# Performance work log

Hardware: AMD Instinct MI355X
Metric: run time of the kernel (lower is better)

Reference implementation:

```python
import jax, jax.numpy as jnp
import numpy as np

B, S, T, E, H = 64, 128, 128, 1024, 1024
NEG = -1e9  # masked-score fill


def setup_inputs() -> dict:
    key = jax.random.key(0)
    ks = jax.random.split(key, 10)
    sd = lambda k, shape, fan: (jax.random.normal(k, shape, jnp.float32) * (fan ** -0.5))
    return {
        "trg_embed": jax.random.normal(ks[0], (B, T, E), jnp.float32),
        "encoder_hidden": jax.random.normal(ks[1], (B, S, 2 * H), jnp.float32),
        "encoder_final": jax.random.normal(ks[2], (1, B, 2 * H), jnp.float32),
        "src_mask": jnp.ones((B, 1, S), bool),
        "trg_mask": jnp.ones((B, T), bool),
        "W_bridge": sd(ks[3], (H, 2 * H), 2 * H),
        "b_bridge": jnp.zeros((H,), jnp.float32),
        "W_key": sd(ks[4], (H, 2 * H), 2 * H),
        "W_query": sd(ks[5], (H, H), H),
        "W_energy": sd(ks[6], (1, H), H),
        "W_ih": sd(ks[7], (3 * H, E + 2 * H), E + 2 * H),
        "W_hh": sd(ks[8], (3 * H, H), H),
        "b_ih": jnp.zeros((3 * H,), jnp.float32),
        "b_hh": jnp.zeros((3 * H,), jnp.float32),
        "W_pre": sd(ks[9], (2 * H, E + 3 * H), E + 3 * H),
    }


def _decode(trg_embed, encoder_hidden, encoder_final, src_mask,
            W_bridge, b_bridge, W_key, W_query, W_energy,
            W_ih, W_hh, b_ih, b_hh, W_pre):
    # init_hidden: tanh(bridge(encoder_final))  -> [num_layers=1, B, H]
    h0 = jnp.tanh(encoder_final @ W_bridge.T + b_bridge)
    # proj_key computed once over the source  -> [B, S, H]
    proj_key = encoder_hidden @ W_key.T
    mask = src_mask[:, 0, :]  # [B, S]
    Hd = W_hh.shape[1]

    def step(hidden, x_t):  # hidden: [1,B,H], x_t: [B,E]
        h = hidden[-1]
        # Bahdanau attention
        q = h @ W_query.T                                   # [B,H]
        scores = jnp.tanh(q[:, None, :] + proj_key) @ W_energy[0]  # [B,S]
        scores = jnp.where(mask, scores, NEG)
        alphas = jax.nn.softmax(scores, axis=-1)
        context = jnp.einsum('bs,bsd->bd', alphas, encoder_hidden)  # [B,2H]
        # GRU cell (PyTorch gate math)
        x = jnp.concatenate([x_t, context], axis=-1)        # [B, E+2H]
        gi = x @ W_ih.T + b_ih
        gh = h @ W_hh.T + b_hh
        r = jax.nn.sigmoid(gi[:, :Hd] + gh[:, :Hd])
        z = jax.nn.sigmoid(gi[:, Hd:2 * Hd] + gh[:, Hd:2 * Hd])
        n = jnp.tanh(gi[:, 2 * Hd:] + r * gh[:, 2 * Hd:])
        h_new = (1.0 - z) * n + z * h
        # pre-output (dropout is identity in eval)
        pre = jnp.concatenate([x_t, h_new, context], axis=-1) @ W_pre.T  # [B,2H]
        return h_new[None], (h_new, pre)

    hidden_final, (outs, pres) = jax.lax.scan(step, h0, jnp.swapaxes(trg_embed, 0, 1))
    decoder_states = jnp.swapaxes(outs, 0, 1)       # [B,T,H]
    pre_output_vectors = jnp.swapaxes(pres, 0, 1)   # [B,T,2H]
    return decoder_states, hidden_final, pre_output_vectors


def reference(trg_embed, encoder_hidden, encoder_final, src_mask, trg_mask,
              W_bridge, b_bridge, W_key, W_query, W_energy,
              W_ih, W_hh, b_ih, b_hh, W_pre):
    # trg_mask only determines max_len, which equals trg_embed.shape[1] here
    return _decode(trg_embed, encoder_hidden, encoder_final, src_mask,
                   W_bridge, b_bridge, W_key, W_query, W_energy,
                   W_ih, W_hh, b_ih, b_hh, W_pre)
```

## Files before the change

kernel.cpp:

```cpp
#include <hip/hip_runtime.h>
#include <hip/hip_bf16.h>

typedef short    bf16x8 __attribute__((ext_vector_type(8)));
typedef float    f32x4  __attribute__((ext_vector_type(4)));
typedef unsigned short u16x8 __attribute__((ext_vector_type(8)));

#define B_  64
#define S_  128
#define T_  128
#define E_  1024
#define H_  1024
#define NBLK 256

#define RLX __ATOMIC_RELAXED
#define AGT __HIP_MEMORY_SCOPE_AGENT

__device__ __forceinline__ unsigned short f2bf(float f) {
    unsigned u = __float_as_uint(f);
    unsigned r = (u + 0x7FFFu + ((u >> 16) & 1u)) >> 16;
    return (unsigned short)r;
}
__device__ __forceinline__ float bf2f(unsigned short u) {
    return __uint_as_float((unsigned)u << 16);
}
__device__ __forceinline__ float my_tanh(float x) {
    float e = __expf(2.0f * x);
    return 1.0f - 2.0f / (e + 1.0f);
}
__device__ __forceinline__ float my_sig(float x) {
    return 1.0f / (1.0f + __expf(-x));
}

__device__ __forceinline__ void st8c(void* p, unsigned long long v) {
    __hip_atomic_store((unsigned long long*)p, v, RLX, AGT);
}
__device__ __forceinline__ unsigned long long ld8c(const void* p) {
    return __hip_atomic_load((const unsigned long long*)p, RLX, AGT);
}
__device__ __forceinline__ void st4c(void* p, unsigned v) {
    __hip_atomic_store((unsigned*)p, v, RLX, AGT);
}
__device__ __forceinline__ void st4f(void* p, float v) {
    __hip_atomic_store((float*)p, v, RLX, AGT);
}
__device__ __forceinline__ float ld4f(const void* p) {
    return __hip_atomic_load((const float*)p, RLX, AGT);
}

__device__ __forceinline__ void gld_lds16(const void* g, void* l) {
    __builtin_amdgcn_global_load_lds(
        (const __attribute__((address_space(1))) unsigned int*)(unsigned long long)g,
        (__attribute__((address_space(3))) unsigned int*)(unsigned int)(unsigned long long)l,
        16, 0, 0);
}

__device__ __forceinline__ void gbar(int* sync, int g, int ord) {
    __syncthreads();
    if (threadIdx.x == 0) {
        int* lc = sync + 64 + (g >> 3) * 64;
        int* lg = lc + 32;
        if (__hip_atomic_fetch_add(lc, 1, RLX, AGT) == 8 * ord - 1) {
            if (__hip_atomic_fetch_add(sync, 1, RLX, AGT) == 32 * ord - 1) {
                __hip_atomic_store(sync + 32, ord, RLX, AGT);
            } else {
                while (__hip_atomic_load(sync + 32, RLX, AGT) < ord)
                    __builtin_amdgcn_s_sleep(2);
            }
            __hip_atomic_store(lg, ord, RLX, AGT);
        } else {
            while (__hip_atomic_load(lg, RLX, AGT) < ord)
                __builtin_amdgcn_s_sleep(2);
        }
    }
    __syncthreads();
}

__global__ void k_cvt(const float* __restrict__ s, unsigned short* __restrict__ d, long n) {
    long i = ((long)blockIdx.x * blockDim.x + threadIdx.x) * 4;
    if (i >= n) return;
    float4 f = *(const float4*)(s + i);
    ushort4 o;
    o.x = f2bf(f.x); o.y = f2bf(f.y); o.z = f2bf(f.z); o.w = f2bf(f.w);
    *(ushort4*)(d + i) = o;
}

__global__ void k_cvt_te(const float* __restrict__ s, unsigned short* __restrict__ d, long n) {
    long i = ((long)blockIdx.x * blockDim.x + threadIdx.x) * 4;
    if (i >= n) return;
    float4 f = *(const float4*)(s + i);
    long row = i >> 10, col = i & 1023;
    ushort4 o;
    o.x = f2bf(f.x); o.y = f2bf(f.y); o.z = f2bf(f.z); o.w = f2bf(f.w);
    *(ushort4*)(d + row * 4096 + col) = o;
}

template<int OUTBF>
__global__ __launch_bounds__(256) void k_gemm(const unsigned short* __restrict__ A, long lda,
                                              const unsigned short* __restrict__ W, long ldw,
                                              void* __restrict__ Cv, long ldc, int K) {
    const int lane = threadIdx.x & 63;
    const int wv   = threadIdx.x >> 6;
    const int r    = lane & 15, g = lane >> 4;
    const long m0  = (long)blockIdx.y * 64 + wv * 16;
    const long n0  = (long)blockIdx.x * 64;
    const unsigned short* a  = A + (m0 + r) * lda + g * 8;
    const unsigned short* w0 = W + (n0 + r) * ldw + g * 8;
    f32x4 acc[4] = {};
    for (int k = 0; k < K; k += 32) {
        bf16x8 av = *(const bf16x8*)(a + k);
#pragma unroll
        for (int j = 0; j < 4; ++j) {
            bf16x8 bv = *(const bf16x8*)(w0 + (long)j * 16 * ldw + k);
            acc[j] = __builtin_amdgcn_mfma_f32_16x16x32_bf16(av, bv, acc[j], 0, 0, 0);
        }
    }
#pragma unroll
    for (int j = 0; j < 4; ++j) {
        long row = m0 + g * 4;
        long col = n0 + j * 16 + r;
#pragma unroll
        for (int rr = 0; rr < 4; ++rr) {
            float v = acc[j][rr];
            if (OUTBF) ((unsigned short*)Cv)[(row + rr) * ldc + col] = f2bf(v);
            else       ((float*)Cv)[(row + rr) * ldc + col] = v;
        }
    }
}

template<int OUTBF>
__global__ __launch_bounds__(256) void k_gemm128(const unsigned short* __restrict__ A, long lda,
                                                 const unsigned short* __restrict__ W, long ldw,
                                                 void* __restrict__ Cv, long ldc, int K) {
    __shared__ unsigned short lA[128 * 32];
    __shared__ unsigned short lB[128 * 32];
    const int tid  = threadIdx.x;
    const int lane = tid & 63, wv = tid >> 6;
    const int r = lane & 15, gg = lane >> 4;
    const int wm = (wv >> 1) * 64, wn = (wv & 1) * 64;
    const long m0 = (long)blockIdx.y * 128;
    const long n0 = (long)blockIdx.x * 128;
    const int c0 = 2 * wv, c1 = 2 * wv + 1;
    const int ra0 = c0 * 16 + (lane >> 2);
    const int ra1 = c1 * 16 + (lane >> 2);
    const int cb8 = (lane & 3) * 8;
    const unsigned short* a0 = A + (m0 + ra0) * lda + cb8;
    const unsigned short* a1 = A + (m0 + ra1) * lda + cb8;
    const unsigned short* b0 = W + (n0 + ra0) * ldw + cb8;
    const unsigned short* b1 = W + (n0 + ra1) * ldw + cb8;
    f32x4 acc[4][4] = {};
    for (int k0 = 0; k0 < K; k0 += 32) {
        __syncthreads();
        gld_lds16(a0 + k0, &lA[c0 * 512]);
        gld_lds16(a1 + k0, &lA[c1 * 512]);
        gld_lds16(b0 + k0, &lB[c0 * 512]);
        gld_lds16(b1 + k0, &lB[c1 * 512]);
        __syncthreads();
        bf16x8 av[4], bv[4];
#pragma unroll
        for (int i = 0; i < 4; ++i) {
            av[i] = *(const bf16x8*)&lA[(wm + i * 16 + r) * 32 + gg * 8];
            bv[i] = *(const bf16x8*)&lB[(wn + i * 16 + r) * 32 + gg * 8];
        }
#pragma unroll
        for (int mi = 0; mi < 4; ++mi)
#pragma unroll
            for (int ni = 0; ni < 4; ++ni)
                acc[mi][ni] = __builtin_amdgcn_mfma_f32_16x16x32_bf16(av[mi], bv[ni], acc[mi][ni], 0, 0, 0);
    }
#pragma unroll
    for (int mi = 0; mi < 4; ++mi) {
#pragma unroll
        for (int ni = 0; ni < 4; ++ni) {
            const long col = n0 + wn + ni * 16 + r;
#pragma unroll
            for (int rr = 0; rr < 4; ++rr) {
                const long row = m0 + wm + mi * 16 + gg * 4 + rr;
                float v = acc[mi][ni][rr];
                if (OUTBF) ((unsigned short*)Cv)[row * ldc + col] = f2bf(v);
                else       ((float*)Cv)[row * ldc + col] = v;
            }
        }
    }
}

__global__ void k_h0act(const float* __restrict__ hp, const float* __restrict__ bb,
                        float* __restrict__ h, unsigned short* __restrict__ hbf) {
    int i = blockIdx.x * 256 + threadIdx.x;
    float v = my_tanh(hp[i] + bb[i & 1023]);
    h[i] = v; hbf[i] = f2bf(v);
}

__global__ __launch_bounds__(1024) void k_steps(
        const unsigned short* __restrict__ pk, const unsigned short* __restrict__ eh,
        const unsigned short* __restrict__ whp, const unsigned short* __restrict__ wih,
        const float* __restrict__ We, const float* __restrict__ gix,
        const float* __restrict__ bih, const float* __restrict__ bhh,
        const float* __restrict__ h0f, const unsigned short* __restrict__ hbf,
        float* __restrict__ hp, unsigned short* __restrict__ preC,
        float* __restrict__ o_states, float* __restrict__ o_hf,
        int* __restrict__ sync, float* __restrict__ scb) {
    __shared__ unsigned short ehs[S_ * 512];
    __shared__ float smf[16 * 64 * 4];
    __shared__ unsigned short hsm[256];
    const int g    = blockIdx.x;
    const int tid  = threadIdx.x;
    const int wv   = tid >> 6, lane = tid & 63;
    const int r    = lane & 15, gg = lane >> 4;

    const int p1_bq = g & 3, p1_cb = g >> 2;
    const int p1_ct = wv & 3, p1_ks = wv >> 2;
    const int p2_b  = (g & 7) * 8 + (g >> 5);
    const int p2_q4 = (g >> 3) & 3;
    const int jt = g >> 2, bg = g & 3;
    const int j0 = jt * 16, b0 = bg * 16;
    const int lr = tid >> 4, lc = tid & 15;
    float hreg = (tid < 256) ? h0f[(long)(b0 + lr) * 1024 + j0 + lc] : 0.f;

    {
        const unsigned short* src = eh + (long)p2_b * S_ * 2048 + p2_q4 * 512;
#pragma unroll
        for (int it = 0; it < 8; ++it) {
            int i = it * 1024 + tid;
            int row = i >> 6, c8i = (i & 63) * 8;
            *(u16x8*)&ehs[row * 512 + c8i] = *(const u16x8*)(src + (long)row * 2048 + c8i);
        }
    }
    __syncthreads();

    int ord = 0;

#pragma unroll 1
    for (int t = 0; t < T_; ++t) {
        {
            const int n0 = p1_cb * 64 + p1_ct * 16;
            const int k0 = p1_ks * 256;
            const int b  = p1_bq * 16 + r;
            const unsigned short* arow = (t == 0)
                ? hbf + (long)b * 1024 + k0 + gg * 8
                : preC + ((long)b * T_ + (t - 1)) * 4096 + 1024 + k0 + gg * 8;
            const unsigned short* bw = whp + (long)(n0 + r) * 1024 + k0 + gg * 8;
            f32x4 acc = {};
#pragma unroll
            for (int k = 0; k < 256; k += 32) {
                bf16x8 av = *(const bf16x8*)(arow + k);
                bf16x8 bv = *(const bf16x8*)(bw + k);
                acc = __builtin_amdgcn_mfma_f32_16x16x32_bf16(av, bv, acc, 0, 0, 0);
            }
            *(f32x4*)&smf[(wv * 64 + lane) * 4] = acc;
            __syncthreads();
            if (p1_ks == 0) {
                f32x4 s0 = *(f32x4*)&smf[((0 * 4 + p1_ct) * 64 + lane) * 4];
                f32x4 s1 = *(f32x4*)&smf[((1 * 4 + p1_ct) * 64 + lane) * 4];
                f32x4 s2 = *(f32x4*)&smf[((2 * 4 + p1_ct) * 64 + lane) * 4];
                f32x4 s3 = *(f32x4*)&smf[((3 * 4 + p1_ct) * 64 + lane) * 4];
                f32x4 s = s0 + s1 + s2 + s3;
#pragma unroll
                for (int rr = 0; rr < 4; ++rr)
                    st4f(&hp[(long)(p1_bq * 16 + gg * 4 + rr) * 4096 + n0 + r], s[rr]);
            }
        }
        gbar(sync, g, ++ord);

        {
            const int b = p2_b;
            const int hh = lane * 16;
            float q[16], w16[16];
#pragma unroll
            for (int i = 0; i < 8; ++i) {
                unsigned long long u = ld8c(hp + (long)b * 4096 + hh + 2 * i);
                q[2 * i]     = __uint_as_float((unsigned)u);
                q[2 * i + 1] = __uint_as_float((unsigned)(u >> 32));
            }
#pragma unroll
            for (int i = 0; i < 16; ++i) w16[i] = We[hh + i];
#pragma unroll
            for (int k2 = 0; k2 < 2; ++k2) {
                const int s = p2_q4 * 32 + wv * 2 + k2;
                const unsigned short* row = pk + ((long)b * S_ + s) * 1024 + hh;
                u16x8 v0 = *(const u16x8*)(row);
                u16x8 v1 = *(const u16x8*)(row + 8);
                float acc = 0.f;
#pragma unroll
                for (int i = 0; i < 8; ++i) acc += my_tanh(q[i] + bf2f(v0[i])) * w16[i];
#pragma unroll
                for (int i = 0; i < 8; ++i) acc += my_tanh(q[8 + i] + bf2f(v1[i])) * w16[8 + i];
#pragma unroll
                for (int off = 32; off; off >>= 1) acc += __shfl_xor(acc, off);
                if (lane == 0) st4f(&scb[b * 128 + s], acc);
            }
            __syncthreads();
            if (tid == 0) {
                int* bc = sync + 4096 + b * 32;
                __hip_atomic_fetch_add(bc, 1, RLX, AGT);
                while (__hip_atomic_load(bc, RLX, AGT) < 4 * (t + 1))
                    __builtin_amdgcn_s_sleep(2);
            }
            __syncthreads();
            float* red = &smf[648];
            float e = 0.f, sc = 0.f;
            if (tid < 128) {
                sc = ld4f(&scb[b * 128 + tid]);
                float m = sc;
#pragma unroll
                for (int off = 32; off; off >>= 1) m = fmaxf(m, __shfl_xor(m, off));
                if ((tid & 63) == 0) red[tid >> 6] = m;
            }
            __syncthreads();
            if (tid < 128) {
                float M = fmaxf(red[0], red[1]);
                e = __expf(sc - M);
                float s = e;
#pragma unroll
                for (int off = 32; off; off >>= 1) s += __shfl_xor(s, off);
                if ((tid & 63) == 0) red[2 + (tid >> 6)] = s;
            }
            __syncthreads();
            if (tid < 128) smf[512 + tid] = e / (red[2] + red[3]);
            __syncthreads();
            const int cp = tid & 255, sseg = tid >> 8;
            const unsigned short* ehp = ehs + (sseg * 32) * 512 + cp * 2;
            float a0 = 0.f, a1 = 0.f;
#pragma unroll 4
            for (int s2 = 0; s2 < 32; ++s2) {
                float alv = smf[512 + sseg * 32 + s2];
                ushort2 v = *(const ushort2*)(ehp + s2 * 512);
                a0 += alv * bf2f(v.x); a1 += alv * bf2f(v.y);
            }
            smf[1024 + (sseg * 256 + cp) * 2]     = a0;
            smf[1024 + (sseg * 256 + cp) * 2 + 1] = a1;
            __syncthreads();
            if (tid < 256) {
                float b0s = smf[1024 + tid * 2]         + smf[1024 + (256 + tid) * 2]
                          + smf[1024 + (512 + tid) * 2] + smf[1024 + (768 + tid) * 2];
                float b1s = smf[1024 + tid * 2 + 1]         + smf[1024 + (256 + tid) * 2 + 1]
                          + smf[1024 + (512 + tid) * 2 + 1] + smf[1024 + (768 + tid) * 2 + 1];
                unsigned pack = (unsigned)f2bf(b0s) | ((unsigned)f2bf(b1s) << 16);
                st4c(preC + ((long)b * T_ + t) * 4096 + 2048 + p2_q4 * 512 + tid * 2, pack);
            }
        }
        gbar(sync, g, ++ord);

        {
            if (wv < 12) {
                const int c = wv >> 2, ks = wv & 3, k0 = ks * 512;
                const unsigned short* ar = preC + ((long)(b0 + r) * T_ + t) * 4096 + 2048 + k0 + gg * 8;
                const unsigned short* bw = wih + ((long)(c * 1024 + j0 + r)) * 3072 + 1024 + k0 + gg * 8;
                f32x4 acc = {};
#pragma unroll
                for (int k = 0; k < 512; k += 32) {
                    bf16x8 av = *(const bf16x8*)(ar + k);
                    bf16x8 bv = *(const bf16x8*)(bw + k);
                    acc = __builtin_amdgcn_mfma_f32_16x16x32_bf16(av, bv, acc, 0, 0, 0);
                }
                *(f32x4*)&smf[(wv * 64 + lane) * 4] = acc;
            }
            __syncthreads();
            if (tid < 256) {
                const int lane_ = (lr >> 2) * 16 + lc, rr_ = lr & 3;
                float gi[3];
#pragma unroll
                for (int c = 0; c < 3; ++c) {
                    gi[c] = smf[((c * 4 + 0) * 64 + lane_) * 4 + rr_]
                          + smf[((c * 4 + 1) * 64 + lane_) * 4 + rr_]
                          + smf[((c * 4 + 2) * 64 + lane_) * 4 + rr_]
                          + smf[((c * 4 + 3) * 64 + lane_) * 4 + rr_];
                }
                const int b = b0 + lr, j = j0 + lc;
                const long bt = (long)b * T_ + t;
                float ghr = ld4f(&hp[(long)b * 4096 + 1024 + j]);
                float ghz = ld4f(&hp[(long)b * 4096 + 2048 + j]);
                float ghn = ld4f(&hp[(long)b * 4096 + 3072 + j]);
                float grv = gix[bt * 3072 + j]        + gi[0] + bih[j]        + ghr + bhh[j];
                float gzv = gix[bt * 3072 + 1024 + j] + gi[1] + bih[1024 + j] + ghz + bhh[1024 + j];
                float gni = gix[bt * 3072 + 2048 + j] + gi[2] + bih[2048 + j];
                float ghn2 = ghn + bhh[2048 + j];
                float rg = my_sig(grv);
                float zg = my_sig(gzv);
                float nv = my_tanh(gni + rg * ghn2);
                float hn = (1.f - zg) * nv + zg * hreg;
                hreg = hn;
                unsigned short hb16 = f2bf(hn);
                o_states[bt * 1024 + j] = hn;
                if (t == T_ - 1) o_hf[(long)b * 1024 + j] = hn;
                hsm[tid] = hb16;
            }
            __syncthreads();
            if (tid < 64) {
                const int plr = tid >> 2, pc4 = (tid & 3) * 4;
                unsigned long long v =
                      (unsigned long long)hsm[plr * 16 + pc4]
                    | ((unsigned long long)hsm[plr * 16 + pc4 + 1] << 16)
                    | ((unsigned long long)hsm[plr * 16 + pc4 + 2] << 32)
                    | ((unsigned long long)hsm[plr * 16 + pc4 + 3] << 48);
                st8c(preC + ((long)(b0 + plr) * T_ + t) * 4096 + 1024 + j0 + pc4, v);
            }
        }
        gbar(sync, g, ++ord);
    }
}

extern "C" void kernel_launch(void* const* d_in, const int* in_sizes, int n_in,
                              void* d_out, int out_size, void* d_ws, size_t ws_size,
                              hipStream_t stream) {
    const float* te  = (const float*)d_in[0];
    const float* eh  = (const float*)d_in[1];
    const float* ef  = (const float*)d_in[2];
    const float* Wb  = (const float*)d_in[5];
    const float* bb  = (const float*)d_in[6];
    const float* Wk  = (const float*)d_in[7];
    const float* Wq  = (const float*)d_in[8];
    const float* We  = (const float*)d_in[9];
    const float* Wih = (const float*)d_in[10];
    const float* Whh = (const float*)d_in[11];
    const float* bih = (const float*)d_in[12];
    const float* bhh = (const float*)d_in[13];
    const float* Wpre= (const float*)d_in[14];

    char* ws = (char*)d_ws;
    if (ws_size < 272236544UL) return;
    float*          h0f   = (float*)(ws + 0);
    float*          hp    = (float*)(ws + 262144);
    unsigned short* hbf   = (unsigned short*)(ws + 1310720);
    unsigned short* efb   = (unsigned short*)(ws + 1441792);
    int*            syncb = (int*)(ws + 1441792 + 65536);
    float*          scb   = (float*)(ws + 1572864);
    unsigned short* ehb   = (unsigned short*)(ws + 1703936);
    unsigned short* pkb   = (unsigned short*)(ws + 35258368);
    unsigned short* preC  = (unsigned short*)(ws + 52035584);
    float*          gix   = (float*)(ws + 119144448);
    unsigned short* wbb   = (unsigned short*)(ws + 219807744);
    unsigned short* wkb   = (unsigned short*)(ws + 224002048);
    unsigned short* whpb  = (unsigned short*)(ws + 228196352);
    unsigned short* wihb  = (unsigned short*)(ws + 236584960);
    unsigned short* wpreb = (unsigned short*)(ws + 255459328);

    float* o_states = (float*)d_out;
    float* o_hf     = o_states + (long)B_ * T_ * H_;
    float* o_pre    = o_hf + (long)B_ * H_;

    auto cvt = [&](const float* s, unsigned short* d, long n) {
        k_cvt<<<dim3((unsigned)((n / 4 + 255) / 256)), 256, 0, stream>>>(s, d, n);
    };
    cvt(eh,  ehb,  (long)B_ * S_ * 2048);
    cvt(ef,  efb,  (long)B_ * 2048);
    cvt(Wb,  wbb,  1024L * 2048);
    cvt(Wk,  wkb,  1024L * 2048);
    cvt(Wq,  whpb, 1024L * 1024);
    cvt(Whh, whpb + 1024L * 1024, 3072L * 1024);
    cvt(Wih, wihb, 3072L * 3072);
    cvt(Wpre,wpreb,2048L * 4096);
    k_cvt_te<<<8192, 256, 0, stream>>>(te, preC, (long)B_ * T_ * 1024);

    k_gemm<0><<<dim3(16, 1), 256, 0, stream>>>(efb, 2048, wbb, 2048, hp, 1024, 2048);
    k_h0act<<<256, 256, 0, stream>>>(hp, bb, h0f, hbf);
    (void)hipMemsetAsync(syncb, 0, 32768, stream);
    k_gemm128<1><<<dim3(8, 64), 256, 0, stream>>>(ehb, 2048, wkb, 2048, pkb, 1024, 2048);
    k_gemm128<0><<<dim3(24, 64), 256, 0, stream>>>(preC, 4096, wihb, 3072, gix, 3072, 1024);

    k_steps<<<NBLK, 1024, 0, stream>>>(pkb, ehb, whpb, wihb, We, gix, bih, bhh,
                                       h0f, hbf, hp, preC, o_states, o_hf, syncb, scb);

    k_gemm128<0><<<dim3(16, 64), 256, 0, stream>>>(preC, 4096, wpreb, 4096, o_pre, 2048, 4096);
}
```

Measured before the change: 5.467 ms.

## Split query and W_hh projections, replace grid barrier with per-batch-group flags

Phase 1 now runs only the query projection (h@W_query) on 64 blocks and writes it to a small qbuf. Each block then signals a per-batch-group counter instead of entering a full grid barrier. The recurrent W_hh gate products move into the GRU phase, where spare waves 12-14 compute them locally over the full K=1024. This removes one global barrier per step and the hp round-trip for the gh terms. In exchange, a few waves per block do a longer serial MFMA loop, and attention blocks spin-wait on counters.

```diff
diff --git a/kernel.cpp b/kernel.cpp
--- a/kernel.cpp
+++ b/kernel.cpp
@@ -196,7 +196,7 @@
         const float* __restrict__ We, const float* __restrict__ gix,
         const float* __restrict__ bih, const float* __restrict__ bhh,
         const float* __restrict__ h0f, const unsigned short* __restrict__ hbf,
-        float* __restrict__ hp, unsigned short* __restrict__ preC,
+        float* __restrict__ qbuf, unsigned short* __restrict__ preC,
         float* __restrict__ o_states, float* __restrict__ o_hf,
         int* __restrict__ sync, float* __restrict__ scb) {
     __shared__ unsigned short ehs[S_ * 512];
@@ -207,8 +207,8 @@
     const int wv   = tid >> 6, lane = tid & 63;
     const int r    = lane & 15, gg = lane >> 4;
 
-    const int p1_bq = g & 3, p1_cb = g >> 2;
-    const int p1_ct = wv & 3, p1_ks = wv >> 2;
+    const int p1_bq = g >> 4, p1_ct = g & 15;
+    const int p1_nt = wv & 3, p1_ks = wv >> 2;
     const int p2_b  = (g & 7) * 8 + (g >> 5);
     const int p2_q4 = (g >> 3) & 3;
     const int jt = g >> 2, bg = g & 3;
@@ -231,8 +231,8 @@
 
 #pragma unroll 1
     for (int t = 0; t < T_; ++t) {
-        {
-            const int n0 = p1_cb * 64 + p1_ct * 16;
+        if (g < 64) {
+            const int n0 = p1_ct * 64 + p1_nt * 16;
             const int k0 = p1_ks * 256;
             const int b  = p1_bq * 16 + r;
             const unsigned short* arow = (t == 0)
@@ -249,25 +249,33 @@
             *(f32x4*)&smf[(wv * 64 + lane) * 4] = acc;
             __syncthreads();
             if (p1_ks == 0) {
-                f32x4 s0 = *(f32x4*)&smf[((0 * 4 + p1_ct) * 64 + lane) * 4];
-                f32x4 s1 = *(f32x4*)&smf[((1 * 4 + p1_ct) * 64 + lane) * 4];
-                f32x4 s2 = *(f32x4*)&smf[((2 * 4 + p1_ct) * 64 + lane) * 4];
-                f32x4 s3 = *(f32x4*)&smf[((3 * 4 + p1_ct) * 64 + lane) * 4];
+                f32x4 s0 = *(f32x4*)&smf[((0 * 4 + p1_nt) * 64 + lane) * 4];
+                f32x4 s1 = *(f32x4*)&smf[((1 * 4 + p1_nt) * 64 + lane) * 4];
+                f32x4 s2 = *(f32x4*)&smf[((2 * 4 + p1_nt) * 64 + lane) * 4];
+                f32x4 s3 = *(f32x4*)&smf[((3 * 4 + p1_nt) * 64 + lane) * 4];
                 f32x4 s = s0 + s1 + s2 + s3;
 #pragma unroll
                 for (int rr = 0; rr < 4; ++rr)
-                    st4f(&hp[(long)(p1_bq * 16 + gg * 4 + rr) * 4096 + n0 + r], s[rr]);
-            }
-        }
-        gbar(sync, g, ++ord);
+                    st4f(&qbuf[(long)(p1_bq * 16 + gg * 4 + rr) * 1024 + n0 + r], s[rr]);
+            }
+            __syncthreads();
+            if (tid == 0)
+                __hip_atomic_fetch_add(sync + 6656 + p1_bq * 32, 1, RLX, AGT);
+        }
 
         {
             const int b = p2_b;
+            if (tid == 0) {
+                int* qc = sync + 6656 + (b >> 4) * 32;
+                while (__hip_atomic_load(qc, RLX, AGT) < 16 * (t + 1))
+                    __builtin_amdgcn_s_sleep(2);
+            }
+            __syncthreads();
             const int hh = lane * 16;
             float q[16], w16[16];
 #pragma unroll
             for (int i = 0; i < 8; ++i) {
-                unsigned long long u = ld8c(hp + (long)b * 4096 + hh + 2 * i);
+                unsigned long long u = ld8c(qbuf + (long)b * 1024 + hh + 2 * i);
                 q[2 * i]     = __uint_as_float((unsigned)u);
                 q[2 * i + 1] = __uint_as_float((unsigned)(u >> 32));
             }
@@ -353,27 +361,39 @@
                     acc = __builtin_amdgcn_mfma_f32_16x16x32_bf16(av, bv, acc, 0, 0, 0);
                 }
                 *(f32x4*)&smf[(wv * 64 + lane) * 4] = acc;
+            } else if (wv < 15) {
+                const int c = wv - 12;
+                const unsigned short* ar = (t == 0)
+                    ? hbf + (long)(b0 + r) * 1024 + gg * 8
+                    : preC + ((long)(b0 + r) * T_ + (t - 1)) * 4096 + 1024 + gg * 8;
+                const unsigned short* bw = whp + (long)(1024 + c * 1024 + j0 + r) * 1024 + gg * 8;
+                f32x4 acc = {};
+#pragma unroll 4
+                for (int k = 0; k < 1024; k += 32) {
+                    bf16x8 av = *(const bf16x8*)(ar + k);
+                    bf16x8 bv = *(const bf16x8*)(bw + k);
+                    acc = __builtin_amdgcn_mfma_f32_16x16x32_bf16(av, bv, acc, 0, 0, 0);
+                }
+                *(f32x4*)&smf[(wv * 64 + lane) * 4] = acc;
             }
             __syncthreads();
             if (tid < 256) {
                 const int lane_ = (lr >> 2) * 16 + lc, rr_ = lr & 3;
-                float gi[3];
+                float gi[3], gh[3];
 #pragma unroll
                 for (int c = 0; c < 3; ++c) {
                     gi[c] = smf[((c * 4 + 0) * 64 + lane_) * 4 + rr_]
                           + smf[((c * 4 + 1) * 64 + lane_) * 4 + rr_]
                           + smf[((c * 4 + 2) * 64 + lane_) * 4 + rr_]
                           + smf[((c * 4 + 3) * 64 + lane_) * 4 + rr_];
+                    gh[c] = smf[((12 + c) * 64 + lane_) * 4 + rr_];
                 }
                 const int b = b0 + lr, j = j0 + lc;
                 const long bt = (long)b * T_ + t;
-                float ghr = ld4f(&hp[(long)b * 4096 + 1024 + j]);
-                float ghz = ld4f(&hp[(long)b * 4096 + 2048 + j]);
-                float ghn = ld4f(&hp[(long)b * 4096 + 3072 + j]);
-                float grv = gix[bt * 3072 + j]        + gi[0] + bih[j]        + ghr + bhh[j];
-                float gzv = gix[bt * 3072 + 1024 + j] + gi[1] + bih[1024 + j] + ghz + bhh[1024 + j];
+                float grv = gix[bt * 3072 + j]        + gi[0] + bih[j]        + gh[0] + bhh[j];
+                float gzv = gix[bt * 3072 + 1024 + j] + gi[1] + bih[1024 + j] + gh[1] + bhh[1024 + j];
                 float gni = gix[bt * 3072 + 2048 + j] + gi[2] + bih[2048 + j];
-                float ghn2 = ghn + bhh[2048 + j];
+                float ghn2 = gh[2] + bhh[2048 + j];
                 float rg = my_sig(grv);
                 float zg = my_sig(gzv);
                 float nv = my_tanh(gni + rg * ghn2);
```

Result: slower. 6.059 ms (+10.8%).

## Split persistent-kernel grid barrier into independent per-batch-quarter barriers

Applied to the files above, without the earlier changes.

Reassigns the 256 persistent blocks so that each group of 64 blocks handles one 16-row batch quarter in every phase (hidden projection, attention, GRU update). The full-grid barrier becomes a 64-block barrier per batch quarter, with its own counters, so the quarters advance through time steps independently. This is meant to shrink barrier fan-in and let slower quarters avoid stalling the whole grid. The block-to-data mapping also groups blocks by XCD index, and the sync buffer clear is doubled to cover the extra counters.

```diff
diff --git a/kernel.cpp b/kernel.cpp
--- a/kernel.cpp
+++ b/kernel.cpp
@@ -47,32 +47,32 @@
     return __hip_atomic_load((const float*)p, RLX, AGT);
 }
 
+__device__ __forceinline__ void gbarq(int* s, int leaf, int ord) {
+    __syncthreads();
+    if (threadIdx.x == 0) {
+        int* lc = s + 64 + leaf * 64;
+        int* lg = lc + 32;
+        if (__hip_atomic_fetch_add(lc, 1, RLX, AGT) == 8 * ord - 1) {
+            if (__hip_atomic_fetch_add(s, 1, RLX, AGT) == 8 * ord - 1) {
+                __hip_atomic_store(s + 32, ord, RLX, AGT);
+            } else {
+                while (__hip_atomic_load(s + 32, RLX, AGT) < ord)
+                    __builtin_amdgcn_s_sleep(2);
+            }
+            __hip_atomic_store(lg, ord, RLX, AGT);
+        } else {
+            while (__hip_atomic_load(lg, RLX, AGT) < ord)
+                __builtin_amdgcn_s_sleep(2);
+        }
+    }
+    __syncthreads();
+}
+
 __device__ __forceinline__ void gld_lds16(const void* g, void* l) {
     __builtin_amdgcn_global_load_lds(
         (const __attribute__((address_space(1))) unsigned int*)(unsigned long long)g,
         (__attribute__((address_space(3))) unsigned int*)(unsigned int)(unsigned long long)l,
         16, 0, 0);
-}
-
-__device__ __forceinline__ void gbar(int* sync, int g, int ord) {
-    __syncthreads();
-    if (threadIdx.x == 0) {
-        int* lc = sync + 64 + (g >> 3) * 64;
-        int* lg = lc + 32;
-        if (__hip_atomic_fetch_add(lc, 1, RLX, AGT) == 8 * ord - 1) {
-            if (__hip_atomic_fetch_add(sync, 1, RLX, AGT) == 32 * ord - 1) {
-                __hip_atomic_store(sync + 32, ord, RLX, AGT);
-            } else {
-                while (__hip_atomic_load(sync + 32, RLX, AGT) < ord)
-                    __builtin_amdgcn_s_sleep(2);
-            }
-            __hip_atomic_store(lg, ord, RLX, AGT);
-        } else {
-            while (__hip_atomic_load(lg, RLX, AGT) < ord)
-                __builtin_amdgcn_s_sleep(2);
-        }
-    }
-    __syncthreads();
 }
 
 __global__ void k_cvt(const float* __restrict__ s, unsigned short* __restrict__ d, long n) {
@@ -207,12 +207,15 @@
     const int wv   = tid >> 6, lane = tid & 63;
     const int r    = lane & 15, gg = lane >> 4;
 
-    const int p1_bq = g & 3, p1_cb = g >> 2;
+    const int bq  = g >> 6, z = g & 63;
+    const int xcd = z & 7, sub = z >> 3;
+    int* bqs = sync + bq * 1024;
+    const int p1_cb = xcd * 8 + sub;
     const int p1_ct = wv & 3, p1_ks = wv >> 2;
-    const int p2_b  = (g & 7) * 8 + (g >> 5);
-    const int p2_q4 = (g >> 3) & 3;
-    const int jt = g >> 2, bg = g & 3;
-    const int j0 = jt * 16, b0 = bg * 16;
+    const int p2_b  = bq * 16 + xcd * 2 + (sub & 1);
+    const int p2_q4 = sub >> 1;
+    const int jt = xcd * 8 + sub;
+    const int j0 = jt * 16, b0 = bq * 16;
     const int lr = tid >> 4, lc = tid & 15;
     float hreg = (tid < 256) ? h0f[(long)(b0 + lr) * 1024 + j0 + lc] : 0.f;
 
@@ -234,7 +237,7 @@
         {
             const int n0 = p1_cb * 64 + p1_ct * 16;
             const int k0 = p1_ks * 256;
-            const int b  = p1_bq * 16 + r;
+            const int b  = bq * 16 + r;
             const unsigned short* arow = (t == 0)
                 ? hbf + (long)b * 1024 + k0 + gg * 8
                 : preC + ((long)b * T_ + (t - 1)) * 4096 + 1024 + k0 + gg * 8;
@@ -256,10 +259,10 @@
                 f32x4 s = s0 + s1 + s2 + s3;
 #pragma unroll
                 for (int rr = 0; rr < 4; ++rr)
-                    st4f(&hp[(long)(p1_bq * 16 + gg * 4 + rr) * 4096 + n0 + r], s[rr]);
-            }
-        }
-        gbar(sync, g, ++ord);
+                    st4f(&hp[(long)(bq * 16 + gg * 4 + rr) * 4096 + n0 + r], s[rr]);
+            }
+        }
+        gbarq(bqs, xcd, ++ord);
 
         {
             const int b = p2_b;
@@ -338,7 +341,7 @@
                 st4c(preC + ((long)b * T_ + t) * 4096 + 2048 + p2_q4 * 512 + tid * 2, pack);
             }
         }
-        gbar(sync, g, ++ord);
+        gbarq(bqs, xcd, ++ord);
 
         {
             if (wv < 12) {
@@ -395,7 +398,7 @@
                 st8c(preC + ((long)(b0 + plr) * T_ + t) * 4096 + 1024 + j0 + pc4, v);
             }
         }
-        gbar(sync, g, ++ord);
+        gbarq(bqs, xcd, ++ord);
     }
 }
 
@@ -453,7 +456,7 @@
 
     k_gemm<0><<<dim3(16, 1), 256, 0, stream>>>(efb, 2048, wbb, 2048, hp, 1024, 2048);
     k_h0act<<<256, 256, 0, stream>>>(hp, bb, h0f, hbf);
-    (void)hipMemsetAsync(syncb, 0, 32768, stream);
+    (void)hipMemsetAsync(syncb, 0, 65536, stream);
     k_gemm128<1><<<dim3(8, 64), 256, 0, stream>>>(ehb, 2048, wkb, 2048, pkb, 1024, 2048);
     k_gemm128<0><<<dim3(24, 64), 256, 0, stream>>>(preC, 4096, wihb, 3072, gix, 3072, 1024);
 
```

Result: faster. 5.102 ms (-6.7%).
